# Kernel optimization log

Measured on AMD Instinct MI355X. Metric: run time of the kernel, lower is better.

## Reference

```python
import jax, jax.numpy as jnp
import numpy as np

S = 1.0   # scale s
M = 0.4   # margin m
EPS = 1e-12  # F.normalize eps


def _l2norm_rows(a):
    # F.normalize(a, dim=1): row-wise L2 normalization
    n = jnp.linalg.norm(a, axis=1, keepdims=True)
    return a / jnp.maximum(n, EPS)


def _half_loss(sim):
    # unique-label branch: positive is the diagonal, all off-diagonal are negatives
    N = sim.shape[0]
    num = S * (jnp.diagonal(sim) - M)                       # [N]
    offdiag = jnp.exp(S * sim) * (1.0 - jnp.eye(N, dtype=sim.dtype))
    denom = jnp.exp(num) + jnp.sum(offdiag, axis=1)         # [N]
    return num - jnp.log(denom)


def setup_inputs() -> dict:
    key = jax.random.key(0)
    k1, k2 = jax.random.split(key)
    N, D = 8192, 256
    return {
        "x1": jax.random.normal(k1, (N, D), dtype=jnp.float32),
        "x2": jax.random.normal(k2, (N, D), dtype=jnp.float32),
        "sentence_id": jnp.arange(N, dtype=jnp.int32),  # unique labels -> more_label=False branch
    }


def reference(x1, x2, sentence_id):
    # x12[i,j] row-normalized similarity of x1_i against all x2_j (and symmetric)
    x12 = _l2norm_rows(x1 @ x2.T)   # [N, N]
    x21 = _l2norm_rows(x2 @ x1.T)   # [N, N]
    L12 = _half_loss(x12)
    L21 = _half_loss(x21)
    loss = -jnp.mean(L12) - jnp.mean(L21)
    return loss, L12, L21
```

## Files before the change

kernel.cpp:

```cpp
#include <hip/hip_runtime.h>
#include <cstdint>
#include <cstddef>


#define NROWS 8192
#define DIMK 256
#define MARGIN 0.4f
#define LOG2E 1.4426950408889634f

typedef short short8 __attribute__((ext_vector_type(8)));
typedef float f32x4 __attribute__((ext_vector_type(4)));

__device__ __forceinline__ unsigned short f2bf(float f) {
  union { float f; unsigned u; } v; v.f = f;
  unsigned r = (v.u + 0x7fffu + ((v.u >> 16) & 1u)) >> 16;
  return (unsigned short)r;
}

__device__ __forceinline__ void gl_lds16(const void* g, void* l) {
  __builtin_amdgcn_global_load_lds((const __attribute__((address_space(1))) void*)g,
                                   (__attribute__((address_space(3))) void*)l, 16, 0, 0);
}

__global__ __launch_bounds__(256)
void k_conv_diag(const float* __restrict__ x1, const float* __restrict__ x2,
                 unsigned short* __restrict__ Ab, unsigned short* __restrict__ Bb,
                 float* __restrict__ diag) {
  const int row = blockIdx.x * 4 + (threadIdx.x >> 6);
  const int l = threadIdx.x & 63;
  const float4 a = ((const float4*)(x1 + (size_t)row * DIMK))[l];
  const float4 b = ((const float4*)(x2 + (size_t)row * DIMK))[l];
  ushort4 ua, ub;
  ua.x = f2bf(a.x); ua.y = f2bf(a.y); ua.z = f2bf(a.z); ua.w = f2bf(a.w);
  ub.x = f2bf(b.x); ub.y = f2bf(b.y); ub.z = f2bf(b.z); ub.w = f2bf(b.w);
  ((ushort4*)(Ab + (size_t)row * DIMK))[l] = ua;
  ((ushort4*)(Bb + (size_t)row * DIMK))[l] = ub;
  float d = a.x * b.x + a.y * b.y + a.z * b.z + a.w * b.w;
#pragma unroll
  for (int m = 1; m < 64; m <<= 1) d += __shfl_xor(d, m);
  if (l == 0) diag[row] = d;
}

__global__ __launch_bounds__(256)
void k_syrk(const unsigned short* __restrict__ Ab, const unsigned short* __restrict__ Bb,
            float* __restrict__ M1, float* __restrict__ M2) {
  __shared__ unsigned short As[64 * 32];
  __shared__ unsigned short Bs[64 * 32];
  const int t = threadIdx.x, w = t >> 6, l = t & 63, quad = l >> 4, l15 = l & 15;
  const int mat = blockIdx.z & 1;
  const int kseg = blockIdx.z >> 1;
  const unsigned short* X = mat ? Bb : Ab;
  float* Mo = mat ? M2 : M1;
  const int a0 = blockIdx.y * 64, b0 = blockIdx.x * 64;
  const int wr = (w >> 1) * 32, wc = (w & 1) * 32;
  f32x4 acc[2][2] = {};
  const int nn = t & 31, cb = t >> 5;
  const int c0 = cb * 8;
  const int nb = kseg * 512;
  for (int n0 = nb; n0 < nb + 512; n0 += 32) {
    short8 va = *(const short8*)(X + (size_t)(n0 + nn) * DIMK + a0 + c0);
    short8 vb = *(const short8*)(X + (size_t)(n0 + nn) * DIMK + b0 + c0);
#pragma unroll
    for (int i = 0; i < 8; ++i) {
      const int c = c0 + i;
      const int sl = (((nn >> 3) ^ ((c >> 1) & 3)) << 3) + (nn & 7);
      As[c * 32 + sl] = va[i];
      Bs[c * 32 + sl] = vb[i];
    }
    __syncthreads();
    short8 af[2], bg[2];
#pragma unroll
    for (int i = 0; i < 2; ++i) {
      const int ra = wr + i * 16 + l15;
      af[i] = *(const short8*)&As[ra * 32 + ((quad ^ ((ra >> 1) & 3)) << 3)];
      const int rb = wc + i * 16 + l15;
      bg[i] = *(const short8*)&Bs[rb * 32 + ((quad ^ ((rb >> 1) & 3)) << 3)];
    }
#pragma unroll
    for (int i = 0; i < 2; ++i)
#pragma unroll
      for (int j = 0; j < 2; ++j)
        acc[i][j] = __builtin_amdgcn_mfma_f32_16x16x32_bf16(af[i], bg[j], acc[i][j], 0, 0, 0);
    __syncthreads();
  }
#pragma unroll
  for (int i = 0; i < 2; ++i)
#pragma unroll
    for (int j = 0; j < 2; ++j)
#pragma unroll
      for (int r = 0; r < 4; ++r) {
        const int lr = wr + i * 16 + quad * 4 + r;
        const int lc = wc + j * 16 + l15;
        atomicAdd(&Mo[(size_t)(a0 + lr) * 256 + b0 + lc], acc[i][j][r]);
      }
}

__global__ void k_convM(const float* __restrict__ M1, unsigned short* __restrict__ M1b,
                        const float* __restrict__ M2, unsigned short* __restrict__ M2b) {
  const int i = (blockIdx.x * 256 + threadIdx.x) * 2;
  M1b[i] = f2bf(M1[i]); M1b[i + 1] = f2bf(M1[i + 1]);
  M2b[i] = f2bf(M2[i]); M2b[i + 1] = f2bf(M2[i + 1]);
}

template <int EPI>
__global__ __launch_bounds__(256)
void k_gemm(const unsigned short* __restrict__ Abuf, const unsigned short* __restrict__ Bbuf,
            const unsigned short* __restrict__ M1b, const unsigned short* __restrict__ M2b,
            const float* __restrict__ x1, const float* __restrict__ x2,
            float* __restrict__ rowsq, float* __restrict__ colsq,
            float* __restrict__ rowExp, float* __restrict__ colExp) {
  __shared__ unsigned short As[2][4096];
  __shared__ unsigned short Bs[2][4096];
  __shared__ float cRow[128];
  __shared__ float cCol[128];

  const unsigned short* A;
  const unsigned short* B;
  const float* Xf = nullptr;
  float* sq = nullptr;
  if (EPI == 0) {
    if (blockIdx.z == 0) { A = Abuf; B = M2b; Xf = x1; sq = rowsq; }
    else                 { A = Bbuf; B = M1b; Xf = x2; sq = colsq; }
  } else {
    A = Abuf; B = Bbuf;
  }

  const int t = threadIdx.x;
  const int w = t >> 6;
  const int l = t & 63;
  const int quad = l >> 4;
  const int l15 = l & 15;
  const int row0 = blockIdx.x * 128;
  const int col0 = blockIdx.y * 128;
  const int wr = (w >> 1) * 64;
  const int wc = (w & 1) * 64;

  if (EPI == 1) {
    if (t < 128) cRow[t] = LOG2E * rsqrtf(rowsq[row0 + t]);
    else cCol[t - 128] = LOG2E * rsqrtf(colsq[col0 + t - 128]);
  }

  f32x4 acc[4][4] = {};

  const int sr0 = l >> 2;
  const int slot = l & 3;
  const int cA = w * 2, cB = w * 2 + 1;
  const int rA = cA * 16 + sr0, rB = cB * 16 + sr0;
  const int scA = (slot ^ ((rA >> 1) & 3)) << 3;
  const int scB = (slot ^ ((rB >> 1) & 3)) << 3;
  const unsigned short* pA0 = A + (size_t)(row0 + rA) * DIMK + scA;
  const unsigned short* pA1 = A + (size_t)(row0 + rB) * DIMK + scB;
  const unsigned short* pB0 = B + (size_t)(col0 + rA) * DIMK + scA;
  const unsigned short* pB1 = B + (size_t)(col0 + rB) * DIMK + scB;
  const int dA0 = cA * 512 + l * 8, dA1 = cB * 512 + l * 8;

  gl_lds16(pA0, &As[0][dA0]);
  gl_lds16(pA1, &As[0][dA1]);
  gl_lds16(pB0, &Bs[0][dA0]);
  gl_lds16(pB1, &Bs[0][dA1]);

#pragma unroll
  for (int k0 = 0; k0 < 8; ++k0) {
    const int cur = k0 & 1;
    __syncthreads();
    if (k0 < 7) {
      const int nxt = cur ^ 1;
      gl_lds16(pA0 + (k0 + 1) * 32, &As[nxt][dA0]);
      gl_lds16(pA1 + (k0 + 1) * 32, &As[nxt][dA1]);
      gl_lds16(pB0 + (k0 + 1) * 32, &Bs[nxt][dA0]);
      gl_lds16(pB1 + (k0 + 1) * 32, &Bs[nxt][dA1]);
    }
    short8 af[4], bg[4];
#pragma unroll
    for (int i = 0; i < 4; ++i) {
      const int ra = wr + i * 16 + l15;
      af[i] = *(const short8*)&As[cur][ra * 32 + ((quad ^ ((ra >> 1) & 3)) << 3)];
      const int rb = wc + i * 16 + l15;
      bg[i] = *(const short8*)&Bs[cur][rb * 32 + ((quad ^ ((rb >> 1) & 3)) << 3)];
    }
#pragma unroll
    for (int i = 0; i < 4; ++i)
#pragma unroll
      for (int j = 0; j < 4; ++j)
        acc[i][j] = __builtin_amdgcn_mfma_f32_16x16x32_bf16(af[i], bg[j], acc[i][j], 0, 0, 0);
  }

  if (EPI == 0) {
#pragma unroll
    for (int i = 0; i < 4; ++i) {
#pragma unroll
      for (int r = 0; r < 4; ++r) {
        const int lr = wr + i * 16 + quad * 4 + r;
        const float* xr = Xf + (size_t)(row0 + lr) * DIMK + col0 + wc;
        float rp = 0.f;
#pragma unroll
        for (int j = 0; j < 4; ++j) rp += acc[i][j][r] * xr[j * 16 + l15];
        rp += __shfl_xor(rp, 1); rp += __shfl_xor(rp, 2);
        rp += __shfl_xor(rp, 4); rp += __shfl_xor(rp, 8);
        if (l15 == 0) atomicAdd(&sq[row0 + lr], rp);
      }
    }
  } else {
    float cj[4];
#pragma unroll
    for (int j = 0; j < 4; ++j) cj[j] = cCol[wc + j * 16 + l15];
    float colpart[4] = {0.f, 0.f, 0.f, 0.f};
#pragma unroll
    for (int i = 0; i < 4; ++i) {
#pragma unroll
      for (int r = 0; r < 4; ++r) {
        const int lr = wr + i * 16 + quad * 4 + r;
        const float ci = cRow[lr];
        float rp = 0.f;
#pragma unroll
        for (int j = 0; j < 4; ++j) {
          const float g = acc[i][j][r];
          rp += __builtin_amdgcn_exp2f(g * ci);
          colpart[j] += __builtin_amdgcn_exp2f(g * cj[j]);
        }
        rp += __shfl_xor(rp, 1); rp += __shfl_xor(rp, 2);
        rp += __shfl_xor(rp, 4); rp += __shfl_xor(rp, 8);
        if (l15 == 0) atomicAdd(&rowExp[row0 + lr], rp);
      }
    }
#pragma unroll
    for (int j = 0; j < 4; ++j) {
      float cp = colpart[j];
      cp += __shfl_xor(cp, 16); cp += __shfl_xor(cp, 32);
      if (l < 16) atomicAdd(&colExp[col0 + wc + j * 16 + l15], cp);
    }
  }
}

__global__ __launch_bounds__(1024)
void k_final(const float* __restrict__ rowsq, const float* __restrict__ colsq,
             const float* __restrict__ diag, const float* __restrict__ rowExp,
             const float* __restrict__ colExp, float* __restrict__ out) {
  const int t = threadIdx.x;
  double part = 0.0;
#pragma unroll
  for (int it = 0; it < 8; ++it) {
    const int i = it * 1024 + t;
    const float d = diag[i];
    const float s1 = d * rsqrtf(rowsq[i]);
    const float s2 = d * rsqrtf(colsq[i]);
    const float n1 = s1 - MARGIN, n2 = s2 - MARGIN;
    const float L1 = n1 - logf(rowExp[i] - expf(s1) + expf(n1));
    const float L2 = n2 - logf(colExp[i] - expf(s2) + expf(n2));
    out[1 + i] = L1;
    out[1 + NROWS + i] = L2;
    part += (double)L1 + (double)L2;
  }
#pragma unroll
  for (int m = 1; m < 64; m <<= 1) part += __shfl_xor(part, m);
  __shared__ double red[16];
  if ((t & 63) == 0) red[t >> 6] = part;
  __syncthreads();
  if (t == 0) {
    double s = 0.0;
#pragma unroll
    for (int i = 0; i < 16; ++i) s += red[i];
    out[0] = (float)(-s / (double)NROWS);
  }
}

extern "C" void kernel_launch(void* const* d_in, const int* in_sizes, int n_in,
                              void* d_out, int out_size, void* d_ws, size_t ws_size,
                              hipStream_t stream) {
  const float* x1 = (const float*)d_in[0];
  const float* x2 = (const float*)d_in[1];
  float* out = (float*)d_out;
  char* ws = (char*)d_ws;

  unsigned short* Ab = (unsigned short*)(ws);
  unsigned short* Bb = (unsigned short*)(ws + 4194304);
  float* M1 = (float*)(ws + 8388608);
  float* M2 = (float*)(ws + 8650752);
  float* rowsq = (float*)(ws + 8912896);
  float* colsq = (float*)(ws + 8945664);
  float* rowExp = (float*)(ws + 8978432);
  float* colExp = (float*)(ws + 9011200);
  unsigned short* M1b = (unsigned short*)(ws + 9043968);
  unsigned short* M2b = (unsigned short*)(ws + 9175040);
  float* diag = (float*)(ws + 9306112);

  hipMemsetAsync(ws + 8388608, 0, 655360, stream);

  k_conv_diag<<<NROWS / 4, 256, 0, stream>>>(x1, x2, Ab, Bb, diag);
  k_syrk<<<dim3(4, 4, 32), 256, 0, stream>>>(Ab, Bb, M1, M2);
  k_convM<<<128, 256, 0, stream>>>(M1, M1b, M2, M2b);
  k_gemm<0><<<dim3(64, 2, 2), 256, 0, stream>>>(Ab, Bb, M1b, M2b, x1, x2,
                                                rowsq, colsq, rowExp, colExp);
  k_gemm<1><<<dim3(64, 64), 256, 0, stream>>>(Ab, Bb, M1b, M2b, x1, x2,
                                              rowsq, colsq, rowExp, colExp);
  k_final<<<1, 1024, 0, stream>>>(rowsq, colsq, diag, rowExp, colExp, out);
}
```

Before: 193.6 us.

## Use 256x256 GEMM tiles with 1024-thread blocks and XCD-aware block mapping

The fused GEMM+exp kernel moves from 128x128 tiles with 256 threads to 256x256 tiles with 1024 threads (16 waves). This halves the global/L2 traffic per output element and cuts the number of row/col atomics. Blocks are remapped so that each XCD handles a contiguous band of column tiles, which should improve L2 locality. The per-row and per-column scale factors are now read directly into registers instead of being staged through LDS, and the final kernel switches to hardware exp2/log intrinsics. The cost is higher LDS use and register pressure per block, with fewer blocks in flight.

```diff
diff --git a/kernel.cpp b/kernel.cpp
--- a/kernel.cpp
+++ b/kernel.cpp
@@ -7,6 +7,7 @@
 #define DIMK 256
 #define MARGIN 0.4f
 #define LOG2E 1.4426950408889634f
+#define LN2 0.6931471805599453f
 
 typedef short short8 __attribute__((ext_vector_type(8)));
 typedef float f32x4 __attribute__((ext_vector_type(4)));
@@ -20,6 +21,10 @@
 __device__ __forceinline__ void gl_lds16(const void* g, void* l) {
   __builtin_amdgcn_global_load_lds((const __attribute__((address_space(1))) void*)g,
                                    (__attribute__((address_space(3))) void*)l, 16, 0, 0);
+}
+
+__device__ __forceinline__ float fexp(float x) {
+  return __builtin_amdgcn_exp2f(x * LOG2E);
 }
 
 __global__ __launch_bounds__(256)
@@ -103,72 +108,60 @@
 }
 
 template <int EPI>
-__global__ __launch_bounds__(256)
+__global__ __launch_bounds__(1024, 4)
 void k_gemm(const unsigned short* __restrict__ Abuf, const unsigned short* __restrict__ Bbuf,
             const unsigned short* __restrict__ M1b, const unsigned short* __restrict__ M2b,
             const float* __restrict__ x1, const float* __restrict__ x2,
             float* __restrict__ rowsq, float* __restrict__ colsq,
             float* __restrict__ rowExp, float* __restrict__ colExp) {
-  __shared__ unsigned short As[2][4096];
-  __shared__ unsigned short Bs[2][4096];
-  __shared__ float cRow[128];
-  __shared__ float cCol[128];
-
+  __shared__ unsigned short As[2][8192];
+  __shared__ unsigned short Bs[2][8192];
+
+  const int t = threadIdx.x;
+  const int w = t >> 6;
+  const int l = t & 63;
+  const int quad = l >> 4;
+  const int l15 = l & 15;
+
+  int row0, col0;
   const unsigned short* A;
   const unsigned short* B;
   const float* Xf = nullptr;
   float* sq = nullptr;
   if (EPI == 0) {
+    row0 = blockIdx.x * 256; col0 = 0;
     if (blockIdx.z == 0) { A = Abuf; B = M2b; Xf = x1; sq = rowsq; }
     else                 { A = Bbuf; B = M1b; Xf = x2; sq = colsq; }
   } else {
+    const int b = blockIdx.x;
+    const int xcd = b & 7;
+    const int s = b >> 3;
+    row0 = (s >> 2) * 256;
+    col0 = (xcd * 4 + (s & 3)) * 256;
     A = Abuf; B = Bbuf;
   }
 
-  const int t = threadIdx.x;
-  const int w = t >> 6;
-  const int l = t & 63;
-  const int quad = l >> 4;
-  const int l15 = l & 15;
-  const int row0 = blockIdx.x * 128;
-  const int col0 = blockIdx.y * 128;
-  const int wr = (w >> 1) * 64;
-  const int wc = (w & 1) * 64;
-
-  if (EPI == 1) {
-    if (t < 128) cRow[t] = LOG2E * rsqrtf(rowsq[row0 + t]);
-    else cCol[t - 128] = LOG2E * rsqrtf(colsq[col0 + t - 128]);
-  }
+  const int wr = (w >> 2) * 64;
+  const int wc = (w & 3) * 64;
 
   f32x4 acc[4][4] = {};
 
-  const int sr0 = l >> 2;
-  const int slot = l & 3;
-  const int cA = w * 2, cB = w * 2 + 1;
-  const int rA = cA * 16 + sr0, rB = cB * 16 + sr0;
-  const int scA = (slot ^ ((rA >> 1) & 3)) << 3;
-  const int scB = (slot ^ ((rB >> 1) & 3)) << 3;
-  const unsigned short* pA0 = A + (size_t)(row0 + rA) * DIMK + scA;
-  const unsigned short* pA1 = A + (size_t)(row0 + rB) * DIMK + scB;
-  const unsigned short* pB0 = B + (size_t)(col0 + rA) * DIMK + scA;
-  const unsigned short* pB1 = B + (size_t)(col0 + rB) * DIMK + scB;
-  const int dA0 = cA * 512 + l * 8, dA1 = cB * 512 + l * 8;
-
-  gl_lds16(pA0, &As[0][dA0]);
-  gl_lds16(pA1, &As[0][dA1]);
-  gl_lds16(pB0, &Bs[0][dA0]);
-  gl_lds16(pB1, &Bs[0][dA1]);
+  const int sr = t >> 2;
+  const int sc = ((t & 3) ^ ((sr >> 1) & 3)) << 3;
+  const unsigned short* pA = A + (size_t)(row0 + sr) * DIMK + sc;
+  const unsigned short* pB = B + (size_t)(col0 + sr) * DIMK + sc;
+  const int dst = t * 8;
+
+  gl_lds16(pA, &As[0][dst]);
+  gl_lds16(pB, &Bs[0][dst]);
 
 #pragma unroll
   for (int k0 = 0; k0 < 8; ++k0) {
     const int cur = k0 & 1;
     __syncthreads();
     if (k0 < 7) {
-      const int nxt = cur ^ 1;
-      gl_lds16(pA0 + (k0 + 1) * 32, &As[nxt][dA0]);
-      gl_lds16(pA1 + (k0 + 1) * 32, &As[nxt][dA1]);
-      gl_lds16(pB0 + (k0 + 1) * 32, &Bs[nxt][dA0]);
-      gl_lds16(pB1 + (k0 + 1) * 32, &Bs[nxt][dA1]);
+      gl_lds16(pA + (k0 + 1) * 32, &As[cur ^ 1][dst]);
+      gl_lds16(pB + (k0 + 1) * 32, &Bs[cur ^ 1][dst]);
     }
     short8 af[4], bg[4];
 #pragma unroll
@@ -203,19 +196,25 @@
   } else {
     float cj[4];
 #pragma unroll
-    for (int j = 0; j < 4; ++j) cj[j] = cCol[wc + j * 16 + l15];
+    for (int j = 0; j < 4; ++j)
+      cj[j] = LOG2E * rsqrtf(colsq[col0 + wc + j * 16 + l15]);
+    float ci[4][4];
+#pragma unroll
+    for (int i = 0; i < 4; ++i)
+#pragma unroll
+      for (int r = 0; r < 4; ++r)
+        ci[i][r] = LOG2E * rsqrtf(rowsq[row0 + wr + i * 16 + quad * 4 + r]);
     float colpart[4] = {0.f, 0.f, 0.f, 0.f};
 #pragma unroll
     for (int i = 0; i < 4; ++i) {
 #pragma unroll
       for (int r = 0; r < 4; ++r) {
         const int lr = wr + i * 16 + quad * 4 + r;
-        const float ci = cRow[lr];
         float rp = 0.f;
 #pragma unroll
         for (int j = 0; j < 4; ++j) {
           const float g = acc[i][j][r];
-          rp += __builtin_amdgcn_exp2f(g * ci);
+          rp += __builtin_amdgcn_exp2f(g * ci[i][r]);
           colpart[j] += __builtin_amdgcn_exp2f(g * cj[j]);
         }
         rp += __shfl_xor(rp, 1); rp += __shfl_xor(rp, 2);
@@ -245,8 +244,8 @@
     const float s1 = d * rsqrtf(rowsq[i]);
     const float s2 = d * rsqrtf(colsq[i]);
     const float n1 = s1 - MARGIN, n2 = s2 - MARGIN;
-    const float L1 = n1 - logf(rowExp[i] - expf(s1) + expf(n1));
-    const float L2 = n2 - logf(colExp[i] - expf(s2) + expf(n2));
+    const float L1 = n1 - LN2 * __builtin_amdgcn_logf(rowExp[i] - fexp(s1) + fexp(n1));
+    const float L2 = n2 - LN2 * __builtin_amdgcn_logf(colExp[i] - fexp(s2) + fexp(n2));
     out[1 + i] = L1;
     out[1 + NROWS + i] = L2;
     part += (double)L1 + (double)L2;
@@ -289,9 +288,9 @@
   k_conv_diag<<<NROWS / 4, 256, 0, stream>>>(x1, x2, Ab, Bb, diag);
   k_syrk<<<dim3(4, 4, 32), 256, 0, stream>>>(Ab, Bb, M1, M2);
   k_convM<<<128, 256, 0, stream>>>(M1, M1b, M2, M2b);
-  k_gemm<0><<<dim3(64, 2, 2), 256, 0, stream>>>(Ab, Bb, M1b, M2b, x1, x2,
-                                                rowsq, colsq, rowExp, colExp);
-  k_gemm<1><<<dim3(64, 64), 256, 0, stream>>>(Ab, Bb, M1b, M2b, x1, x2,
-                                              rowsq, colsq, rowExp, colExp);
+  k_gemm<0><<<dim3(32, 1, 2), 1024, 0, stream>>>(Ab, Bb, M1b, M2b, x1, x2,
+                                                 rowsq, colsq, rowExp, colExp);
+  k_gemm<1><<<dim3(1024, 1, 1), 1024, 0, stream>>>(Ab, Bb, M1b, M2b, x1, x2,
+                                                   rowsq, colsq, rowExp, colExp);
   k_final<<<1, 1024, 0, stream>>>(rowsq, colsq, diag, rowExp, colExp, out);
 }
```

Measured after the change: 233.3 us. 1.2x slower.

## Fuse memset, M conversion and final reduction into neighboring kernels

Applied to the files above, without the earlier changes.

Folds the workspace memset into the prep kernel as extra zeroing blocks, and converts the fp32 M matrices to bf16 directly while staging them in the norm GEMM, which drops the separate k_convM kernel. It also moves the final loss computation into the exp GEMM: per-row-block and per-column-block counters pick the last finishing block, which computes L12/L21 and adds them into a global loss accumulator. This removes three launches and one round trip for the small M buffers. In exchange it adds atomic counters, fences and serialized tail work, and the final mean is now accumulated with float atomics instead of a double reduction.

```diff
diff --git a/kernel.cpp b/kernel.cpp
--- a/kernel.cpp
+++ b/kernel.cpp
@@ -7,6 +7,7 @@
 #define DIMK 256
 #define MARGIN 0.4f
 #define LOG2E 1.4426950408889634f
+#define LN2 0.6931471805599453f
 
 typedef short short8 __attribute__((ext_vector_type(8)));
 typedef float f32x4 __attribute__((ext_vector_type(4)));
@@ -22,23 +23,34 @@
                                    (__attribute__((address_space(3))) void*)l, 16, 0, 0);
 }
 
+__device__ __forceinline__ float fexp(float x) {
+  return __builtin_amdgcn_exp2f(x * LOG2E);
+}
+
 __global__ __launch_bounds__(256)
-void k_conv_diag(const float* __restrict__ x1, const float* __restrict__ x2,
-                 unsigned short* __restrict__ Ab, unsigned short* __restrict__ Bb,
-                 float* __restrict__ diag) {
-  const int row = blockIdx.x * 4 + (threadIdx.x >> 6);
-  const int l = threadIdx.x & 63;
-  const float4 a = ((const float4*)(x1 + (size_t)row * DIMK))[l];
-  const float4 b = ((const float4*)(x2 + (size_t)row * DIMK))[l];
-  ushort4 ua, ub;
-  ua.x = f2bf(a.x); ua.y = f2bf(a.y); ua.z = f2bf(a.z); ua.w = f2bf(a.w);
-  ub.x = f2bf(b.x); ub.y = f2bf(b.y); ub.z = f2bf(b.z); ub.w = f2bf(b.w);
-  ((ushort4*)(Ab + (size_t)row * DIMK))[l] = ua;
-  ((ushort4*)(Bb + (size_t)row * DIMK))[l] = ub;
-  float d = a.x * b.x + a.y * b.y + a.z * b.z + a.w * b.w;
-#pragma unroll
-  for (int m = 1; m < 64; m <<= 1) d += __shfl_xor(d, m);
-  if (l == 0) diag[row] = d;
+void k_prep(const float* __restrict__ x1, const float* __restrict__ x2,
+            unsigned short* __restrict__ Ab, unsigned short* __restrict__ Bb,
+            float* __restrict__ diag, float* __restrict__ zero_region) {
+  const int t = threadIdx.x;
+  if (blockIdx.x < 2048) {
+    const int row = blockIdx.x * 4 + (t >> 6);
+    const int l = t & 63;
+    const float4 a = ((const float4*)(x1 + (size_t)row * DIMK))[l];
+    const float4 b = ((const float4*)(x2 + (size_t)row * DIMK))[l];
+    ushort4 ua, ub;
+    ua.x = f2bf(a.x); ua.y = f2bf(a.y); ua.z = f2bf(a.z); ua.w = f2bf(a.w);
+    ub.x = f2bf(b.x); ub.y = f2bf(b.y); ub.z = f2bf(b.z); ub.w = f2bf(b.w);
+    ((ushort4*)(Ab + (size_t)row * DIMK))[l] = ua;
+    ((ushort4*)(Bb + (size_t)row * DIMK))[l] = ub;
+    float d = a.x * b.x + a.y * b.y + a.z * b.z + a.w * b.w;
+#pragma unroll
+    for (int m = 1; m < 64; m <<= 1) d += __shfl_xor(d, m);
+    if (l == 0) diag[row] = d;
+  } else {
+    const size_t off = (size_t)(blockIdx.x - 2048) * 1024 + t * 4;
+    float4 z = {0.f, 0.f, 0.f, 0.f};
+    *(float4*)(zero_region + off) = z;
+  }
 }
 
 __global__ __launch_bounds__(256)
@@ -95,35 +107,103 @@
       }
 }
 
-__global__ void k_convM(const float* __restrict__ M1, unsigned short* __restrict__ M1b,
-                        const float* __restrict__ M2, unsigned short* __restrict__ M2b) {
-  const int i = (blockIdx.x * 256 + threadIdx.x) * 2;
-  M1b[i] = f2bf(M1[i]); M1b[i + 1] = f2bf(M1[i + 1]);
-  M2b[i] = f2bf(M2[i]); M2b[i + 1] = f2bf(M2[i + 1]);
-}
-
-template <int EPI>
 __global__ __launch_bounds__(256)
-void k_gemm(const unsigned short* __restrict__ Abuf, const unsigned short* __restrict__ Bbuf,
-            const unsigned short* __restrict__ M1b, const unsigned short* __restrict__ M2b,
-            const float* __restrict__ x1, const float* __restrict__ x2,
-            float* __restrict__ rowsq, float* __restrict__ colsq,
-            float* __restrict__ rowExp, float* __restrict__ colExp) {
+void k_gemmN(const unsigned short* __restrict__ Ab, const unsigned short* __restrict__ Bb,
+             const float* __restrict__ M1, const float* __restrict__ M2,
+             const float* __restrict__ x1, const float* __restrict__ x2,
+             float* __restrict__ rowsq, float* __restrict__ colsq) {
+  __shared__ unsigned short As[2][4096];
+  __shared__ unsigned short Bs[2][4096];
+  const int t = threadIdx.x, w = t >> 6, l = t & 63, quad = l >> 4, l15 = l & 15;
+  const unsigned short* A;
+  const float* Mf;
+  const float* Xf;
+  float* sq;
+  if (blockIdx.z == 0) { A = Ab; Mf = M2; Xf = x1; sq = rowsq; }
+  else                 { A = Bb; Mf = M1; Xf = x2; sq = colsq; }
+  const int row0 = blockIdx.x * 128;
+  const int col0 = blockIdx.y * 128;
+  const int wr = (w >> 1) * 64, wc = (w & 1) * 64;
+  f32x4 acc[4][4] = {};
+
+  const int sr0 = l >> 2, slot = l & 3;
+  const int cA = w * 2, cB = w * 2 + 1;
+  const int rA = cA * 16 + sr0, rB = cB * 16 + sr0;
+  const int scA = (slot ^ ((rA >> 1) & 3)) << 3;
+  const int scB = (slot ^ ((rB >> 1) & 3)) << 3;
+  const unsigned short* pA0 = A + (size_t)(row0 + rA) * DIMK + scA;
+  const unsigned short* pA1 = A + (size_t)(row0 + rB) * DIMK + scB;
+  const int dA0 = cA * 512 + l * 8, dA1 = cB * 512 + l * 8;
+
+  auto stageB = [&](int k0, int buf) {
+#pragma unroll
+    for (int g = 0; g < 2; ++g) {
+      const int e = g * 2048 + t * 8;
+      const int c = e >> 5, kk = e & 31;
+      const float4 v0 = *(const float4*)(Mf + (size_t)(col0 + c) * 256 + k0 + kk);
+      const float4 v1 = *(const float4*)(Mf + (size_t)(col0 + c) * 256 + k0 + kk + 4);
+      ushort4 u0, u1;
+      u0.x = f2bf(v0.x); u0.y = f2bf(v0.y); u0.z = f2bf(v0.z); u0.w = f2bf(v0.w);
+      u1.x = f2bf(v1.x); u1.y = f2bf(v1.y); u1.z = f2bf(v1.z); u1.w = f2bf(v1.w);
+      const int sw = ((kk >> 3) ^ ((c >> 1) & 3)) << 3;
+      *(ushort4*)&Bs[buf][c * 32 + sw] = u0;
+      *(ushort4*)&Bs[buf][c * 32 + sw + 4] = u1;
+    }
+  };
+  auto issueA = [&](int k0, int buf) {
+    gl_lds16(pA0 + k0, &As[buf][dA0]);
+    gl_lds16(pA1 + k0, &As[buf][dA1]);
+  };
+
+  stageB(0, 0);
+  issueA(0, 0);
+#pragma unroll
+  for (int k = 0; k < 8; ++k) {
+    const int cur = k & 1;
+    __syncthreads();
+    if (k < 7) { stageB((k + 1) * 32, cur ^ 1); issueA((k + 1) * 32, cur ^ 1); }
+    short8 af[4], bg[4];
+#pragma unroll
+    for (int i = 0; i < 4; ++i) {
+      const int ra = wr + i * 16 + l15;
+      af[i] = *(const short8*)&As[cur][ra * 32 + ((quad ^ ((ra >> 1) & 3)) << 3)];
+      const int rb = wc + i * 16 + l15;
+      bg[i] = *(const short8*)&Bs[cur][rb * 32 + ((quad ^ ((rb >> 1) & 3)) << 3)];
+    }
+#pragma unroll
+    for (int i = 0; i < 4; ++i)
+#pragma unroll
+      for (int j = 0; j < 4; ++j)
+        acc[i][j] = __builtin_amdgcn_mfma_f32_16x16x32_bf16(af[i], bg[j], acc[i][j], 0, 0, 0);
+  }
+
+#pragma unroll
+  for (int i = 0; i < 4; ++i) {
+#pragma unroll
+    for (int r = 0; r < 4; ++r) {
+      const int lr = wr + i * 16 + quad * 4 + r;
+      const float* xr = Xf + (size_t)(row0 + lr) * DIMK + col0 + wc;
+      float rp = 0.f;
+#pragma unroll
+      for (int j = 0; j < 4; ++j) rp += acc[i][j][r] * xr[j * 16 + l15];
+      rp += __shfl_xor(rp, 1); rp += __shfl_xor(rp, 2);
+      rp += __shfl_xor(rp, 4); rp += __shfl_xor(rp, 8);
+      if (l15 == 0) atomicAdd(&sq[row0 + lr], rp);
+    }
+  }
+}
+
+__global__ __launch_bounds__(256)
+void k_gemmE(const unsigned short* __restrict__ Abuf, const unsigned short* __restrict__ Bbuf,
+             const float* __restrict__ rowsq, const float* __restrict__ colsq,
+             float* __restrict__ rowExp, float* __restrict__ colExp,
+             const float* __restrict__ diag, float* __restrict__ lossAcc,
+             int* __restrict__ cntR, int* __restrict__ cntC, int* __restrict__ doneCnt,
+             float* __restrict__ out) {
   __shared__ unsigned short As[2][4096];
   __shared__ unsigned short Bs[2][4096];
   __shared__ float cRow[128];
   __shared__ float cCol[128];
-
-  const unsigned short* A;
-  const unsigned short* B;
-  const float* Xf = nullptr;
-  float* sq = nullptr;
-  if (EPI == 0) {
-    if (blockIdx.z == 0) { A = Abuf; B = M2b; Xf = x1; sq = rowsq; }
-    else                 { A = Bbuf; B = M1b; Xf = x2; sq = colsq; }
-  } else {
-    A = Abuf; B = Bbuf;
-  }
 
   const int t = threadIdx.x;
   const int w = t >> 6;
@@ -135,10 +215,8 @@
   const int wr = (w >> 1) * 64;
   const int wc = (w & 1) * 64;
 
-  if (EPI == 1) {
-    if (t < 128) cRow[t] = LOG2E * rsqrtf(rowsq[row0 + t]);
-    else cCol[t - 128] = LOG2E * rsqrtf(colsq[col0 + t - 128]);
-  }
+  if (t < 128) cRow[t] = LOG2E * rsqrtf(rowsq[row0 + t]);
+  else cCol[t - 128] = LOG2E * rsqrtf(colsq[col0 + t - 128]);
 
   f32x4 acc[4][4] = {};
 
@@ -148,10 +226,10 @@
   const int rA = cA * 16 + sr0, rB = cB * 16 + sr0;
   const int scA = (slot ^ ((rA >> 1) & 3)) << 3;
   const int scB = (slot ^ ((rB >> 1) & 3)) << 3;
-  const unsigned short* pA0 = A + (size_t)(row0 + rA) * DIMK + scA;
-  const unsigned short* pA1 = A + (size_t)(row0 + rB) * DIMK + scB;
-  const unsigned short* pB0 = B + (size_t)(col0 + rA) * DIMK + scA;
-  const unsigned short* pB1 = B + (size_t)(col0 + rB) * DIMK + scB;
+  const unsigned short* pA0 = Abuf + (size_t)(row0 + rA) * DIMK + scA;
+  const unsigned short* pA1 = Abuf + (size_t)(row0 + rB) * DIMK + scB;
+  const unsigned short* pB0 = Bbuf + (size_t)(col0 + rA) * DIMK + scA;
+  const unsigned short* pB1 = Bbuf + (size_t)(col0 + rB) * DIMK + scB;
   const int dA0 = cA * 512 + l * 8, dA1 = cB * 512 + l * 8;
 
   gl_lds16(pA0, &As[0][dA0]);
@@ -185,82 +263,77 @@
         acc[i][j] = __builtin_amdgcn_mfma_f32_16x16x32_bf16(af[i], bg[j], acc[i][j], 0, 0, 0);
   }
 
-  if (EPI == 0) {
-#pragma unroll
-    for (int i = 0; i < 4; ++i) {
-#pragma unroll
-      for (int r = 0; r < 4; ++r) {
-        const int lr = wr + i * 16 + quad * 4 + r;
-        const float* xr = Xf + (size_t)(row0 + lr) * DIMK + col0 + wc;
-        float rp = 0.f;
-#pragma unroll
-        for (int j = 0; j < 4; ++j) rp += acc[i][j][r] * xr[j * 16 + l15];
-        rp += __shfl_xor(rp, 1); rp += __shfl_xor(rp, 2);
-        rp += __shfl_xor(rp, 4); rp += __shfl_xor(rp, 8);
-        if (l15 == 0) atomicAdd(&sq[row0 + lr], rp);
+  float cj[4];
+#pragma unroll
+  for (int j = 0; j < 4; ++j) cj[j] = cCol[wc + j * 16 + l15];
+  float colpart[4] = {0.f, 0.f, 0.f, 0.f};
+#pragma unroll
+  for (int i = 0; i < 4; ++i) {
+#pragma unroll
+    for (int r = 0; r < 4; ++r) {
+      const int lr = wr + i * 16 + quad * 4 + r;
+      const float ci = cRow[lr];
+      float rp = 0.f;
+#pragma unroll
+      for (int j = 0; j < 4; ++j) {
+        const float g = acc[i][j][r];
+        rp += __builtin_amdgcn_exp2f(g * ci);
+        colpart[j] += __builtin_amdgcn_exp2f(g * cj[j]);
       }
-    }
-  } else {
-    float cj[4];
-#pragma unroll
-    for (int j = 0; j < 4; ++j) cj[j] = cCol[wc + j * 16 + l15];
-    float colpart[4] = {0.f, 0.f, 0.f, 0.f};
-#pragma unroll
-    for (int i = 0; i < 4; ++i) {
-#pragma unroll
-      for (int r = 0; r < 4; ++r) {
-        const int lr = wr + i * 16 + quad * 4 + r;
-        const float ci = cRow[lr];
-        float rp = 0.f;
-#pragma unroll
-        for (int j = 0; j < 4; ++j) {
-          const float g = acc[i][j][r];
-          rp += __builtin_amdgcn_exp2f(g * ci);
-          colpart[j] += __builtin_amdgcn_exp2f(g * cj[j]);
-        }
-        rp += __shfl_xor(rp, 1); rp += __shfl_xor(rp, 2);
-        rp += __shfl_xor(rp, 4); rp += __shfl_xor(rp, 8);
-        if (l15 == 0) atomicAdd(&rowExp[row0 + lr], rp);
+      rp += __shfl_xor(rp, 1); rp += __shfl_xor(rp, 2);
+      rp += __shfl_xor(rp, 4); rp += __shfl_xor(rp, 8);
+      if (l15 == 0) atomicAdd(&rowExp[row0 + lr], rp);
+    }
+  }
+#pragma unroll
+  for (int j = 0; j < 4; ++j) {
+    float cp = colpart[j];
+    cp += __shfl_xor(cp, 16); cp += __shfl_xor(cp, 32);
+    if (l < 16) atomicAdd(&colExp[col0 + wc + j * 16 + l15], cp);
+  }
+
+  __threadfence();
+  __shared__ int sOldR, sOldC;
+  if (t == 0) {
+    sOldR = atomicAdd(&cntR[blockIdx.x], 1);
+    sOldC = atomicAdd(&cntC[blockIdx.y], 1);
+  }
+  __syncthreads();
+  const bool doR = (sOldR == 63), doC = (sOldC == 63);
+  if (!doR && !doC) return;
+
+  __shared__ float red[4];
+  for (int side = 0; side < 2; ++side) {
+    if (side == 0 ? !doR : !doC) continue;
+    const int base = side == 0 ? row0 : col0;
+    const float* sq = side == 0 ? rowsq : colsq;
+    float* ex = side == 0 ? rowExp : colExp;
+    float* outp = out + 1 + side * NROWS;
+    float L = 0.f;
+    if (t < 128) {
+      const int i = base + t;
+      const float d = diag[i];
+      const float s = d * rsqrtf(sq[i]);
+      const float n = s - MARGIN;
+      const float E = __hip_atomic_load(&ex[i], __ATOMIC_ACQUIRE, __HIP_MEMORY_SCOPE_AGENT);
+      L = n - LN2 * __builtin_amdgcn_logf(E - fexp(s) + fexp(n));
+      outp[i] = L;
+    }
+    float sum = L;
+#pragma unroll
+    for (int m = 1; m < 64; m <<= 1) sum += __shfl_xor(sum, m);
+    if (l == 0) red[w] = sum;
+    __syncthreads();
+    if (t == 0) {
+      atomicAdd(lossAcc, red[0] + red[1] + red[2] + red[3]);
+      __threadfence();
+      const int od = atomicAdd(doneCnt, 1);
+      if (od == 127) {
+        const float la = __hip_atomic_load(lossAcc, __ATOMIC_ACQUIRE, __HIP_MEMORY_SCOPE_AGENT);
+        out[0] = -la * (1.0f / (float)NROWS);
       }
     }
-#pragma unroll
-    for (int j = 0; j < 4; ++j) {
-      float cp = colpart[j];
-      cp += __shfl_xor(cp, 16); cp += __shfl_xor(cp, 32);
-      if (l < 16) atomicAdd(&colExp[col0 + wc + j * 16 + l15], cp);
-    }
-  }
-}
-
-__global__ __launch_bounds__(1024)
-void k_final(const float* __restrict__ rowsq, const float* __restrict__ colsq,
-             const float* __restrict__ diag, const float* __restrict__ rowExp,
-             const float* __restrict__ colExp, float* __restrict__ out) {
-  const int t = threadIdx.x;
-  double part = 0.0;
-#pragma unroll
-  for (int it = 0; it < 8; ++it) {
-    const int i = it * 1024 + t;
-    const float d = diag[i];
-    const float s1 = d * rsqrtf(rowsq[i]);
-    const float s2 = d * rsqrtf(colsq[i]);
-    const float n1 = s1 - MARGIN, n2 = s2 - MARGIN;
-    const float L1 = n1 - logf(rowExp[i] - expf(s1) + expf(n1));
-    const float L2 = n2 - logf(colExp[i] - expf(s2) + expf(n2));
-    out[1 + i] = L1;
-    out[1 + NROWS + i] = L2;
-    part += (double)L1 + (double)L2;
-  }
-#pragma unroll
-  for (int m = 1; m < 64; m <<= 1) part += __shfl_xor(part, m);
-  __shared__ double red[16];
-  if ((t & 63) == 0) red[t >> 6] = part;
-  __syncthreads();
-  if (t == 0) {
-    double s = 0.0;
-#pragma unroll
-    for (int i = 0; i < 16; ++i) s += red[i];
-    out[0] = (float)(-s / (double)NROWS);
+    __syncthreads();
   }
 }
 
@@ -280,18 +353,16 @@
   float* colsq = (float*)(ws + 8945664);
   float* rowExp = (float*)(ws + 8978432);
   float* colExp = (float*)(ws + 9011200);
-  unsigned short* M1b = (unsigned short*)(ws + 9043968);
-  unsigned short* M2b = (unsigned short*)(ws + 9175040);
-  float* diag = (float*)(ws + 9306112);
-
-  hipMemsetAsync(ws + 8388608, 0, 655360, stream);
-
-  k_conv_diag<<<NROWS / 4, 256, 0, stream>>>(x1, x2, Ab, Bb, diag);
+  char* ctrl = ws + 9043968;
+  float* lossAcc = (float*)(ctrl);
+  int* cntR = (int*)(ctrl + 256);
+  int* cntC = (int*)(ctrl + 512);
+  int* doneCnt = (int*)(ctrl + 768);
+  float* diag = (float*)(ws + 9048064);
+
+  k_prep<<<2209, 256, 0, stream>>>(x1, x2, Ab, Bb, diag, (float*)(ws + 8388608));
   k_syrk<<<dim3(4, 4, 32), 256, 0, stream>>>(Ab, Bb, M1, M2);
-  k_convM<<<128, 256, 0, stream>>>(M1, M1b, M2, M2b);
-  k_gemm<0><<<dim3(64, 2, 2), 256, 0, stream>>>(Ab, Bb, M1b, M2b, x1, x2,
-                                                rowsq, colsq, rowExp, colExp);
-  k_gemm<1><<<dim3(64, 64), 256, 0, stream>>>(Ab, Bb, M1b, M2b, x1, x2,
-                                              rowsq, colsq, rowExp, colExp);
-  k_final<<<1, 1024, 0, stream>>>(rowsq, colsq, diag, rowExp, colExp, out);
-}
+  k_gemmN<<<dim3(64, 2, 2), 256, 0, stream>>>(Ab, Bb, M1, M2, x1, x2, rowsq, colsq);
+  k_gemmE<<<dim3(64, 64), 256, 0, stream>>>(Ab, Bb, rowsq, colsq, rowExp, colExp,
+                                            diag, lossAcc, cntR, cntC, doneCnt, out);
+}
```

Result: slower. 421.2 us (+117.6%).
